# Kernel optimization log

Measured on AMD Instinct MI355X. Metric: run time of the kernel, lower is better.

## Reference

```python
import jax, jax.numpy as jnp
import numpy as np

B, N, D, K = 4, 256, 128, 8
H = 2 * D   # MLP hidden
F3 = 3 * D  # pair feature dim


def setup_inputs() -> dict:
    key = jax.random.key(0)
    ks = jax.random.split(key, 9)
    init = lambda k, shape: (jax.random.normal(k, shape, jnp.float32) * 0.02)
    s = jax.random.normal(ks[0], (B, N, D), jnp.float32)
    return {
        "s": s,
        "Wg1": init(ks[1], (F3, H)), "bg1": jnp.zeros((H,), jnp.float32),
        "Wg2": init(ks[2], (H, 1)),  "bg2": jnp.zeros((1,), jnp.float32),
        "Wa1": init(ks[3], (F3, H)), "ba1": jnp.zeros((H,), jnp.float32),
        "Wa2": init(ks[4], (H, 1)),  "ba2": jnp.zeros((1,), jnp.float32),
    }


def _mlp(x, W1, b1, W2, b2):
    # 2-layer MLP: Linear -> ReLU -> Linear (dropout inactive at eval)
    return jax.nn.relu(x @ W1 + b1) @ W2 + b2


def reference(s, Wg1, bg1, Wg2, bg2, Wa1, ba1, Wa2, ba2):
    b, n, d = s.shape
    si = s[:, :, None, :]                      # [B,N,1,D]
    sj = s[:, None, :, :]                      # [B,1,N,D]
    pair = jnp.concatenate([
        jnp.broadcast_to(si, (b, n, n, d)),
        jnp.broadcast_to(sj, (b, n, n, d)),
        si * sj,
    ], axis=-1)                                # [B,N,N,3D]

    # Stage 1: discrete top-K peer gating
    scores = _mlp(pair, Wg1, bg1, Wg2, bg2)[..., 0]   # [B,N,N]
    k = min(K, n)
    _, topk_idx = jax.lax.top_k(scores, k)            # [B,N,K]
    gate = jax.nn.one_hot(topk_idx, n, dtype=jnp.float32).sum(-2)  # [B,N,N] binary

    # Stage 2: soft relevance weighting over selected peers
    att_logits = _mlp(pair, Wa1, ba1, Wa2, ba2)[..., 0]            # [B,N,N]
    att_logits = jnp.where(gate > 0, att_logits, -jnp.inf)
    att_weights = jnp.nan_to_num(jax.nn.softmax(att_logits, axis=-1))

    ctx = jnp.einsum('bij,bij,bjd->bid', gate, att_weights, s)     # [B,N,D]
    return ctx, gate, att_weights
```

## Files before the change

### kernel.cpp

```cpp
#include <hip/hip_runtime.h>
#include <math.h>

#define B_ 4
#define N_ 256
#define D_ 128
#define H_ 256
#define K_ 8
#define KK 256
#define NJP 64

typedef short v8s __attribute__((ext_vector_type(8)));
typedef float v16f __attribute__((ext_vector_type(16)));

__device__ inline void split_bf16(float x, unsigned short& hi, unsigned short& lo) {
  unsigned u = __float_as_uint(x);
  unsigned uh = u & 0xFFFF0000u;
  hi = (unsigned short)(uh >> 16);
  float r = x - __uint_as_float(uh);
  unsigned ur = __float_as_uint(r);
  ur += 0x7FFFu + ((ur >> 16) & 1u);
  lo = (unsigned short)(ur >> 16);
}

__global__ __launch_bounds__(256) void prep_an(
    const float* __restrict__ s,
    const float* __restrict__ Wg1, const float* __restrict__ bg1,
    const float* __restrict__ Wa1, const float* __restrict__ ba1,
    float* __restrict__ Ag, float* __restrict__ Aa,
    unsigned short* __restrict__ Shi, unsigned short* __restrict__ Slo) {
  const int b = blockIdx.x >> 8;
  const int n = blockIdx.x & 255;
  const int h = threadIdx.x;
  __shared__ float sh[D_];
  if (h < D_) sh[h] = s[(b * N_ + n) * D_ + h];
  __syncthreads();
  float ag = bg1[h], aa = ba1[h];
#pragma unroll 8
  for (int d = 0; d < D_; d++) {
    ag = fmaf(sh[d], Wg1[d * H_ + h], ag);
    aa = fmaf(sh[d], Wa1[d * H_ + h], aa);
  }
  Ag[(b * N_ + n) * H_ + h] = ag;
  Aa[(b * N_ + n) * H_ + h] = aa;
  if (h < D_) {
    unsigned short x, y;
    split_bf16(sh[h], x, y);
    Shi[(b * N_ + n) * D_ + h] = x;
    Slo[(b * N_ + n) * D_ + h] = y;
  }
}

__global__ __launch_bounds__(64) void prep_sw(
    const float* __restrict__ Wg1, const float* __restrict__ Wa1,
    unsigned short* __restrict__ Wghi, unsigned short* __restrict__ Wglo,
    unsigned short* __restrict__ Wahi) {
  const int ks = blockIdx.x >> 3;
  const int tile = blockIdx.x & 7;
  const int lane = threadIdx.x;
  const int h = tile * 32 + (lane & 31);
  const int kbase = ks * 16 + (lane >> 5) * 8;
  const int idx0 = (blockIdx.x * 64 + lane) * 8;
#pragma unroll
  for (int e = 0; e < 8; e++) {
    const int k = kbase + e;
    const int f = (k < D_) ? (2 * D_ + k) : k;
    unsigned short x, y;
    split_bf16(Wg1[f * H_ + h], x, y);
    Wghi[idx0 + e] = x;
    Wglo[idx0 + e] = y;
    unsigned short xa, ya;
    split_bf16(Wa1[f * H_ + h], xa, ya);
    Wahi[idx0 + e] = xa;
  }
}

__global__ __launch_bounds__(256) void prep_sf(
    const unsigned short* __restrict__ Shi, const unsigned short* __restrict__ Slo,
    unsigned short* __restrict__ Sfh, unsigned short* __restrict__ Sfl) {
  const int b = blockIdx.x >> 3, jt = blockIdx.x & 7;
  const int lane = threadIdx.x & 63;
  const int k0 = threadIdx.x >> 6;
  const int j = jt * 32 + (lane & 31);
#pragma unroll
  for (int ksl = k0; ksl < 8; ksl += 4) {
    const int d = ksl * 16 + (lane >> 5) * 8;
    const int src = (b * N_ + j) * D_ + d;
    const int dst = (((b * 8 + jt) * 8 + ksl) * 64 + lane) * 8;
    *(v8s*)(Sfh + dst) = *(const v8s*)(Shi + src);
    *(v8s*)(Sfl + dst) = *(const v8s*)(Slo + src);
  }
}

__device__ inline void arg_better(float v2, int i2, float& v, int& idx) {
  if (v2 > v || (v2 == v && i2 < idx)) { v = v2; idx = i2; }
}

__device__ inline int a_idx(int jl, int k) {
  return (((jl >> 5) * 8 + (k >> 4)) * 64 + ((k >> 3) & 1) * 32 + (jl & 31)) * 8
         + (k & 7);
}
#define ALO 8192

__global__ __launch_bounds__(256, 2) void score_kernel(
    const float* __restrict__ s,
    const float* __restrict__ Ag, const float* __restrict__ Aa,
    const unsigned short* __restrict__ Shi, const unsigned short* __restrict__ Slo,
    const unsigned short* __restrict__ Sfh, const unsigned short* __restrict__ Sfl,
    const unsigned short* __restrict__ Wghi, const unsigned short* __restrict__ Wglo,
    const unsigned short* __restrict__ Wahi,
    const float* __restrict__ Wg2, const float* __restrict__ bg2p,
    const float* __restrict__ Wa2, const float* __restrict__ ba2p,
    float* __restrict__ out) {
  const int b = blockIdx.x >> 8;
  const int i = blockIdx.x & 255;
  const int t = threadIdx.x;
  const int wv = t >> 6, lane = t & 63;
  const int m32 = lane & 31, half32 = lane >> 5;

  __shared__ __align__(16) unsigned short a_all[2 * 8192 + 64];
  __shared__ float si_sh[D_];
  __shared__ float sc_part[8 * NJP];
  __shared__ float scg_sh[N_];
  __shared__ float attl_sh[N_];
  __shared__ float red_v[4];
  __shared__ int red_i[4];
  __shared__ int sel_list[K_];

  if (t < D_) si_sh[t] = s[(b * N_ + i) * D_ + t];

  float agv[2], w2g[2], aav[2], w2a[2];
#pragma unroll
  for (int ht = 0; ht < 2; ht++) {
    const int hg = wv * 64 + ht * 32 + m32;
    agv[ht] = Ag[(b * N_ + i) * H_ + hg];
    w2g[ht] = Wg2[hg];
    aav[ht] = Aa[(b * N_ + i) * H_ + hg];
    w2a[ht] = Wa2[hg];
  }

  const int boff = ((2 * wv) * 64 + lane) * 8;

#pragma unroll 1
  for (int ph = 0; ph < 4; ph++) {
    __syncthreads();
    {
      const int jl = t >> 2, kq = t & 3;
      const int jg = b * N_ + ph * NJP + jl;
      const float* srow = s + jg * D_ + kq * 32;
      const float* sic = si_sh + kq * 32;
#pragma unroll
      for (int u = 0; u < 4; u++) {
        const float4 sv0 = *(const float4*)(srow + u * 8);
        const float4 sv1 = *(const float4*)(srow + u * 8 + 4);
        unsigned short hh[8], ll[8];
        split_bf16(sic[u * 8 + 0] * sv0.x, hh[0], ll[0]);
        split_bf16(sic[u * 8 + 1] * sv0.y, hh[1], ll[1]);
        split_bf16(sic[u * 8 + 2] * sv0.z, hh[2], ll[2]);
        split_bf16(sic[u * 8 + 3] * sv0.w, hh[3], ll[3]);
        split_bf16(sic[u * 8 + 4] * sv1.x, hh[4], ll[4]);
        split_bf16(sic[u * 8 + 5] * sv1.y, hh[5], ll[5]);
        split_bf16(sic[u * 8 + 6] * sv1.z, hh[6], ll[6]);
        split_bf16(sic[u * 8 + 7] * sv1.w, hh[7], ll[7]);
        v8s vh, vl;
#pragma unroll
        for (int e = 0; e < 8; e++) { vh[e] = (short)hh[e]; vl[e] = (short)ll[e]; }
        const int idx = a_idx(jl, kq * 32 + u * 8);
        *(v8s*)(a_all + idx) = vh;
        *(v8s*)(a_all + ALO + idx) = vl;
      }
    }
    __syncthreads();

    const unsigned short* sf_base_h = Sfh + ((b * 8 + ph * 2) * 8) * 512 + lane * 8;
    const unsigned short* sf_base_l = Sfl + ((b * 8 + ph * 2) * 8) * 512 + lane * 8;

    {
      v16f acc[2][2];
#pragma unroll
      for (int jt = 0; jt < 2; jt++)
#pragma unroll
        for (int ht = 0; ht < 2; ht++) acc[jt][ht] = (v16f)(0.f);

      const unsigned short* pgh = Wghi + boff;
      const unsigned short* pgl = Wglo + boff;
      v8s bh[2][2], bl[2][2];
      bh[0][0] = *(const v8s*)pgh;  bh[0][1] = *(const v8s*)(pgh + 512);
      bl[0][0] = *(const v8s*)pgl;  bl[0][1] = *(const v8s*)(pgl + 512);
      pgh += 4096;  pgl += 4096;

      const unsigned short* ahp = a_all + lane * 8;
#pragma unroll 2
      for (int ks = 0; ks < 8; ks++) {
        const int cur = ks & 1, nxt = cur ^ 1;
        bh[nxt][0] = *(const v8s*)pgh;  bh[nxt][1] = *(const v8s*)(pgh + 512);
        bl[nxt][0] = *(const v8s*)pgl;  bl[nxt][1] = *(const v8s*)(pgl + 512);
        pgh += 4096;  pgl += 4096;
        v8s ah0 = *(const v8s*)(ahp);
        v8s ah1 = *(const v8s*)(ahp + 4096);
        v8s al0 = *(const v8s*)(ahp + ALO);
        v8s al1 = *(const v8s*)(ahp + ALO + 4096);
        ahp += 512;
        acc[0][0] = __builtin_amdgcn_mfma_f32_32x32x16_bf16(ah0, bh[cur][0], acc[0][0], 0, 0, 0);
        acc[0][1] = __builtin_amdgcn_mfma_f32_32x32x16_bf16(ah0, bh[cur][1], acc[0][1], 0, 0, 0);
        acc[0][0] = __builtin_amdgcn_mfma_f32_32x32x16_bf16(ah0, bl[cur][0], acc[0][0], 0, 0, 0);
        acc[0][1] = __builtin_amdgcn_mfma_f32_32x32x16_bf16(ah0, bl[cur][1], acc[0][1], 0, 0, 0);
        acc[0][0] = __builtin_amdgcn_mfma_f32_32x32x16_bf16(al0, bh[cur][0], acc[0][0], 0, 0, 0);
        acc[0][1] = __builtin_amdgcn_mfma_f32_32x32x16_bf16(al0, bh[cur][1], acc[0][1], 0, 0, 0);
        acc[1][0] = __builtin_amdgcn_mfma_f32_32x32x16_bf16(ah1, bh[cur][0], acc[1][0], 0, 0, 0);
        acc[1][1] = __builtin_amdgcn_mfma_f32_32x32x16_bf16(ah1, bh[cur][1], acc[1][1], 0, 0, 0);
        acc[1][0] = __builtin_amdgcn_mfma_f32_32x32x16_bf16(ah1, bl[cur][0], acc[1][0], 0, 0, 0);
        acc[1][1] = __builtin_amdgcn_mfma_f32_32x32x16_bf16(ah1, bl[cur][1], acc[1][1], 0, 0, 0);
        acc[1][0] = __builtin_amdgcn_mfma_f32_32x32x16_bf16(al1, bh[cur][0], acc[1][0], 0, 0, 0);
        acc[1][1] = __builtin_amdgcn_mfma_f32_32x32x16_bf16(al1, bh[cur][1], acc[1][1], 0, 0, 0);
      }
      const unsigned short* sfh = sf_base_h;
      const unsigned short* sfl = sf_base_l;
#pragma unroll 2
      for (int ks = 8; ks < 16; ks++) {
        const int cur = ks & 1, nxt = cur ^ 1;
        bh[nxt][0] = *(const v8s*)pgh;  bh[nxt][1] = *(const v8s*)(pgh + 512);
        bl[nxt][0] = *(const v8s*)pgl;  bl[nxt][1] = *(const v8s*)(pgl + 512);
        pgh += 4096;  pgl += 4096;
        v8s ah0 = *(const v8s*)(sfh);
        v8s ah1 = *(const v8s*)(sfh + 4096);
        v8s al0 = *(const v8s*)(sfl);
        v8s al1 = *(const v8s*)(sfl + 4096);
        sfh += 512;  sfl += 512;
        acc[0][0] = __builtin_amdgcn_mfma_f32_32x32x16_bf16(ah0, bh[cur][0], acc[0][0], 0, 0, 0);
        acc[0][1] = __builtin_amdgcn_mfma_f32_32x32x16_bf16(ah0, bh[cur][1], acc[0][1], 0, 0, 0);
        acc[0][0] = __builtin_amdgcn_mfma_f32_32x32x16_bf16(ah0, bl[cur][0], acc[0][0], 0, 0, 0);
        acc[0][1] = __builtin_amdgcn_mfma_f32_32x32x16_bf16(ah0, bl[cur][1], acc[0][1], 0, 0, 0);
        acc[0][0] = __builtin_amdgcn_mfma_f32_32x32x16_bf16(al0, bh[cur][0], acc[0][0], 0, 0, 0);
        acc[0][1] = __builtin_amdgcn_mfma_f32_32x32x16_bf16(al0, bh[cur][1], acc[0][1], 0, 0, 0);
        acc[1][0] = __builtin_amdgcn_mfma_f32_32x32x16_bf16(ah1, bh[cur][0], acc[1][0], 0, 0, 0);
        acc[1][1] = __builtin_amdgcn_mfma_f32_32x32x16_bf16(ah1, bh[cur][1], acc[1][1], 0, 0, 0);
        acc[1][0] = __builtin_amdgcn_mfma_f32_32x32x16_bf16(ah1, bl[cur][0], acc[1][0], 0, 0, 0);
        acc[1][1] = __builtin_amdgcn_mfma_f32_32x32x16_bf16(ah1, bl[cur][1], acc[1][1], 0, 0, 0);
        acc[1][0] = __builtin_amdgcn_mfma_f32_32x32x16_bf16(al1, bh[cur][0], acc[1][0], 0, 0, 0);
        acc[1][1] = __builtin_amdgcn_mfma_f32_32x32x16_bf16(al1, bh[cur][1], acc[1][1], 0, 0, 0);
      }
      float sg[32];
#pragma unroll
      for (int m = 0; m < 32; m++) sg[m] = 0.f;
#pragma unroll
      for (int ht = 0; ht < 2; ht++)
#pragma unroll
        for (int jt = 0; jt < 2; jt++)
#pragma unroll
          for (int r = 0; r < 16; r++) {
            const float z = acc[jt][ht][r] + agv[ht];
            sg[jt * 16 + r] = fmaf(fmaxf(z, 0.f), w2g[ht], sg[jt * 16 + r]);
          }
#pragma unroll
      for (int m = 0; m < 32; m++) {
        float v = sg[m];
#pragma unroll
        for (int off = 1; off <= 16; off <<= 1) v += __shfl_xor(v, off, 64);
        sg[m] = v;
      }
      if (m32 == 0) {
#pragma unroll
        for (int jt = 0; jt < 2; jt++)
#pragma unroll
          for (int r = 0; r < 16; r++) {
            const int jl = jt * 32 + (r & 3) + 8 * (r >> 2) + 4 * half32;
            sc_part[wv * NJP + jl] = sg[jt * 16 + r];
          }
      }
    }

    {
      v16f acc[2][2];
#pragma unroll
      for (int jt = 0; jt < 2; jt++)
#pragma unroll
        for (int ht = 0; ht < 2; ht++) acc[jt][ht] = (v16f)(0.f);

      const unsigned short* pah = Wahi + boff;
      v8s bh[2][2];
      bh[0][0] = *(const v8s*)pah;  bh[0][1] = *(const v8s*)(pah + 512);
      pah += 4096;

      const unsigned short* ahp = a_all + lane * 8;
#pragma unroll 2
      for (int ks = 0; ks < 8; ks++) {
        const int cur = ks & 1, nxt = cur ^ 1;
        bh[nxt][0] = *(const v8s*)pah;  bh[nxt][1] = *(const v8s*)(pah + 512);
        pah += 4096;
        v8s ah0 = *(const v8s*)(ahp);
        v8s ah1 = *(const v8s*)(ahp + 4096);
        ahp += 512;
        acc[0][0] = __builtin_amdgcn_mfma_f32_32x32x16_bf16(ah0, bh[cur][0], acc[0][0], 0, 0, 0);
        acc[0][1] = __builtin_amdgcn_mfma_f32_32x32x16_bf16(ah0, bh[cur][1], acc[0][1], 0, 0, 0);
        acc[1][0] = __builtin_amdgcn_mfma_f32_32x32x16_bf16(ah1, bh[cur][0], acc[1][0], 0, 0, 0);
        acc[1][1] = __builtin_amdgcn_mfma_f32_32x32x16_bf16(ah1, bh[cur][1], acc[1][1], 0, 0, 0);
      }
      const unsigned short* sfh = sf_base_h;
#pragma unroll 2
      for (int ks = 8; ks < 16; ks++) {
        const int cur = ks & 1, nxt = cur ^ 1;
        bh[nxt][0] = *(const v8s*)pah;  bh[nxt][1] = *(const v8s*)(pah + 512);
        pah += 4096;
        v8s ah0 = *(const v8s*)(sfh);
        v8s ah1 = *(const v8s*)(sfh + 4096);
        sfh += 512;
        acc[0][0] = __builtin_amdgcn_mfma_f32_32x32x16_bf16(ah0, bh[cur][0], acc[0][0], 0, 0, 0);
        acc[0][1] = __builtin_amdgcn_mfma_f32_32x32x16_bf16(ah0, bh[cur][1], acc[0][1], 0, 0, 0);
        acc[1][0] = __builtin_amdgcn_mfma_f32_32x32x16_bf16(ah1, bh[cur][0], acc[1][0], 0, 0, 0);
        acc[1][1] = __builtin_amdgcn_mfma_f32_32x32x16_bf16(ah1, bh[cur][1], acc[1][1], 0, 0, 0);
      }
      float sa[32];
#pragma unroll
      for (int m = 0; m < 32; m++) sa[m] = 0.f;
#pragma unroll
      for (int ht = 0; ht < 2; ht++)
#pragma unroll
        for (int jt = 0; jt < 2; jt++)
#pragma unroll
          for (int r = 0; r < 16; r++) {
            const float z = acc[jt][ht][r] + aav[ht];
            sa[jt * 16 + r] = fmaf(fmaxf(z, 0.f), w2a[ht], sa[jt * 16 + r]);
          }
#pragma unroll
      for (int m = 0; m < 32; m++) {
        float v = sa[m];
#pragma unroll
        for (int off = 1; off <= 16; off <<= 1) v += __shfl_xor(v, off, 64);
        sa[m] = v;
      }
      if (m32 == 0) {
#pragma unroll
        for (int jt = 0; jt < 2; jt++)
#pragma unroll
          for (int r = 0; r < 16; r++) {
            const int jl = jt * 32 + (r & 3) + 8 * (r >> 2) + 4 * half32;
            sc_part[4 * NJP + wv * NJP + jl] = sa[jt * 16 + r];
          }
      }
    }
    __syncthreads();
    if (t < NJP) {
      scg_sh[ph * NJP + t] = sc_part[t] + sc_part[NJP + t] + sc_part[2 * NJP + t]
                           + sc_part[3 * NJP + t] + bg2p[0];
      attl_sh[ph * NJP + t] = sc_part[4 * NJP + t] + sc_part[5 * NJP + t]
                            + sc_part[6 * NJP + t] + sc_part[7 * NJP + t] + ba2p[0];
    }
  }
  __syncthreads();

  for (int k = 0; k < K_; k++) {
    float v = scg_sh[t];
    int idx = t;
#pragma unroll
    for (int off = 32; off > 0; off >>= 1) {
      const float vo = __shfl_down(v, off, 64);
      const int io = __shfl_down(idx, off, 64);
      arg_better(vo, io, v, idx);
    }
    if ((t & 63) == 0) { red_v[t >> 6] = v; red_i[t >> 6] = idx; }
    __syncthreads();
    if (t == 0) {
      float bv = red_v[0];
      int bi = red_i[0];
      for (int w = 1; w < 4; w++) arg_better(red_v[w], red_i[w], bv, bi);
      sel_list[k] = bi;
      scg_sh[bi] = -INFINITY;
    }
    __syncthreads();
  }

  bool selj = false;
#pragma unroll
  for (int k = 0; k < K_; k++) selj = selj || (sel_list[k] == t);

  if (t == 0) {
    float m = -INFINITY;
    for (int k = 0; k < K_; k++) m = fmaxf(m, attl_sh[sel_list[k]]);
    float ssum = 0.f;
    for (int k = 0; k < K_; k++) ssum += expf(attl_sh[sel_list[k]] - m);
    red_v[0] = m;
    red_v[1] = ssum;
  }
  __syncthreads();
  const float att = selj ? expf(attl_sh[t] - red_v[0]) / red_v[1] : 0.f;

  float* __restrict__ ctx_out = out;
  float* __restrict__ gate_out = out + B_ * N_ * D_;
  float* __restrict__ att_out = out + B_ * N_ * D_ + B_ * N_ * N_;

  const int row = (b * N_ + i) * N_;
  gate_out[row + t] = selj ? 1.f : 0.f;
  att_out[row + t] = att;

  __syncthreads();
  attl_sh[t] = att;
  __syncthreads();

  if (t < D_) {
    float acc2 = 0.f;
#pragma unroll
    for (int k = 0; k < K_; k++) {
      const int jj = sel_list[k];
      acc2 = fmaf(attl_sh[jj], s[(b * N_ + jj) * D_ + t], acc2);
    }
    ctx_out[(b * N_ + i) * D_ + t] = acc2;
  }
}

extern "C" void kernel_launch(void* const* d_in, const int* in_sizes, int n_in,
                              void* d_out, int out_size, void* d_ws, size_t ws_size,
                              hipStream_t stream) {
  const float* s   = (const float*)d_in[0];
  const float* Wg1 = (const float*)d_in[1];
  const float* bg1 = (const float*)d_in[2];
  const float* Wg2 = (const float*)d_in[3];
  const float* bg2 = (const float*)d_in[4];
  const float* Wa1 = (const float*)d_in[5];
  const float* ba1 = (const float*)d_in[6];
  const float* Wa2 = (const float*)d_in[7];
  const float* ba2 = (const float*)d_in[8];
  float* out = (float*)d_out;

  float* ws = (float*)d_ws;
  float* Ag = ws;
  float* Aa = Ag + B_ * N_ * H_;
  unsigned short* Shi  = (unsigned short*)(Aa + B_ * N_ * H_);
  unsigned short* Slo  = Shi + B_ * N_ * D_;
  unsigned short* Wghi = Slo + B_ * N_ * D_;
  unsigned short* Wglo = Wghi + 65536 + 4096;
  unsigned short* Wahi = Wglo + 65536 + 4096;
  unsigned short* Sfh  = Wahi + 65536 + 4096;
  unsigned short* Sfl  = Sfh + B_ * 32768;

  prep_an<<<dim3(B_ * N_), dim3(256), 0, stream>>>(
      s, Wg1, bg1, Wa1, ba1, Ag, Aa, Shi, Slo);
  prep_sw<<<dim3(128), dim3(64), 0, stream>>>(Wg1, Wa1, Wghi, Wglo, Wahi);
  prep_sf<<<dim3(B_ * 8), dim3(256), 0, stream>>>(Shi, Slo, Sfh, Sfl);
  score_kernel<<<dim3(B_ * N_), dim3(256), 0, stream>>>(
      s, Ag, Aa, Shi, Slo, Sfh, Sfl, Wghi, Wglo, Wahi, Wg2, bg2, Wa2, ba2, out);
}
```

Measured before the change: 264.5 us.

## Process two query rows per score block and merge prep kernels into one

Each score_kernel block now handles two query rows i, so the per-j weight fragments (Wg/Wa hi/lo) and the Sf tiles loaded from global memory are reused across two sets of MFMA accumulators. This halves the grid to 512 blocks and doubles the accumulator registers and shared-memory A buffers. The three prep kernels are fused into a single launch, and the split of s into bf16 hi/lo is done directly from fp32 inside it, removing the Shi/Slo intermediates. The risks are higher register pressure under launch_bounds(256,2), which could cause spills or lower occupancy, and fewer blocks to spread across the CUs.

```diff
diff --git a/kernel.cpp b/kernel.cpp
--- a/kernel.cpp
+++ b/kernel.cpp
@@ -6,7 +6,6 @@
 #define D_ 128
 #define H_ 256
 #define K_ 8
-#define KK 256
 #define NJP 64
 
 typedef short v8s __attribute__((ext_vector_type(8)));
@@ -22,72 +21,73 @@
   lo = (unsigned short)(ur >> 16);
 }
 
-__global__ __launch_bounds__(256) void prep_an(
+__global__ __launch_bounds__(256) void prep_all(
     const float* __restrict__ s,
     const float* __restrict__ Wg1, const float* __restrict__ bg1,
     const float* __restrict__ Wa1, const float* __restrict__ ba1,
     float* __restrict__ Ag, float* __restrict__ Aa,
-    unsigned short* __restrict__ Shi, unsigned short* __restrict__ Slo) {
-  const int b = blockIdx.x >> 8;
-  const int n = blockIdx.x & 255;
-  const int h = threadIdx.x;
+    unsigned short* __restrict__ Wghi, unsigned short* __restrict__ Wglo,
+    unsigned short* __restrict__ Wahi,
+    unsigned short* __restrict__ Sfh, unsigned short* __restrict__ Sfl) {
   __shared__ float sh[D_];
-  if (h < D_) sh[h] = s[(b * N_ + n) * D_ + h];
-  __syncthreads();
-  float ag = bg1[h], aa = ba1[h];
+  const int blk = blockIdx.x;
+  if (blk < 1024) {
+    const int b = blk >> 8, n = blk & 255, h = threadIdx.x;
+    if (h < D_) sh[h] = s[(b * N_ + n) * D_ + h];
+    __syncthreads();
+    float ag = bg1[h], aa = ba1[h];
 #pragma unroll 8
-  for (int d = 0; d < D_; d++) {
-    ag = fmaf(sh[d], Wg1[d * H_ + h], ag);
-    aa = fmaf(sh[d], Wa1[d * H_ + h], aa);
-  }
-  Ag[(b * N_ + n) * H_ + h] = ag;
-  Aa[(b * N_ + n) * H_ + h] = aa;
-  if (h < D_) {
-    unsigned short x, y;
-    split_bf16(sh[h], x, y);
-    Shi[(b * N_ + n) * D_ + h] = x;
-    Slo[(b * N_ + n) * D_ + h] = y;
-  }
-}
-
-__global__ __launch_bounds__(64) void prep_sw(
-    const float* __restrict__ Wg1, const float* __restrict__ Wa1,
-    unsigned short* __restrict__ Wghi, unsigned short* __restrict__ Wglo,
-    unsigned short* __restrict__ Wahi) {
-  const int ks = blockIdx.x >> 3;
-  const int tile = blockIdx.x & 7;
-  const int lane = threadIdx.x;
-  const int h = tile * 32 + (lane & 31);
-  const int kbase = ks * 16 + (lane >> 5) * 8;
-  const int idx0 = (blockIdx.x * 64 + lane) * 8;
-#pragma unroll
-  for (int e = 0; e < 8; e++) {
-    const int k = kbase + e;
-    const int f = (k < D_) ? (2 * D_ + k) : k;
-    unsigned short x, y;
-    split_bf16(Wg1[f * H_ + h], x, y);
-    Wghi[idx0 + e] = x;
-    Wglo[idx0 + e] = y;
-    unsigned short xa, ya;
-    split_bf16(Wa1[f * H_ + h], xa, ya);
-    Wahi[idx0 + e] = xa;
-  }
-}
-
-__global__ __launch_bounds__(256) void prep_sf(
-    const unsigned short* __restrict__ Shi, const unsigned short* __restrict__ Slo,
-    unsigned short* __restrict__ Sfh, unsigned short* __restrict__ Sfl) {
-  const int b = blockIdx.x >> 3, jt = blockIdx.x & 7;
-  const int lane = threadIdx.x & 63;
-  const int k0 = threadIdx.x >> 6;
-  const int j = jt * 32 + (lane & 31);
-#pragma unroll
-  for (int ksl = k0; ksl < 8; ksl += 4) {
-    const int d = ksl * 16 + (lane >> 5) * 8;
-    const int src = (b * N_ + j) * D_ + d;
-    const int dst = (((b * 8 + jt) * 8 + ksl) * 64 + lane) * 8;
-    *(v8s*)(Sfh + dst) = *(const v8s*)(Shi + src);
-    *(v8s*)(Sfl + dst) = *(const v8s*)(Slo + src);
+    for (int d = 0; d < D_; d++) {
+      ag = fmaf(sh[d], Wg1[d * H_ + h], ag);
+      aa = fmaf(sh[d], Wa1[d * H_ + h], aa);
+    }
+    Ag[(b * N_ + n) * H_ + h] = ag;
+    Aa[(b * N_ + n) * H_ + h] = aa;
+  } else if (blk < 1152) {
+    const int id = blk - 1024;
+    if (threadIdx.x < 64) {
+      const int ks = id >> 3, tile = id & 7, lane = threadIdx.x;
+      const int h = tile * 32 + (lane & 31);
+      const int kbase = ks * 16 + (lane >> 5) * 8;
+      const int idx0 = (id * 64 + lane) * 8;
+#pragma unroll
+      for (int e = 0; e < 8; e++) {
+        const int k = kbase + e;
+        const int f = (k < D_) ? (2 * D_ + k) : k;
+        unsigned short x, y;
+        split_bf16(Wg1[f * H_ + h], x, y);
+        Wghi[idx0 + e] = x;
+        Wglo[idx0 + e] = y;
+        unsigned short xa, ya;
+        split_bf16(Wa1[f * H_ + h], xa, ya);
+        Wahi[idx0 + e] = xa;
+      }
+    }
+  } else {
+    const int id = blk - 1152;
+    const int b = id >> 3, jt = id & 7;
+    const int lane = threadIdx.x & 63, k0 = threadIdx.x >> 6;
+    const int j = jt * 32 + (lane & 31);
+#pragma unroll
+    for (int ksl = k0; ksl < 8; ksl += 4) {
+      const int d = ksl * 16 + (lane >> 5) * 8;
+      const float* sp = s + (b * N_ + j) * D_ + d;
+      const float4 f0 = *(const float4*)(sp);
+      const float4 f1 = *(const float4*)(sp + 4);
+      v8s vh, vl;
+      unsigned short x, y;
+      split_bf16(f0.x, x, y); vh[0] = (short)x; vl[0] = (short)y;
+      split_bf16(f0.y, x, y); vh[1] = (short)x; vl[1] = (short)y;
+      split_bf16(f0.z, x, y); vh[2] = (short)x; vl[2] = (short)y;
+      split_bf16(f0.w, x, y); vh[3] = (short)x; vl[3] = (short)y;
+      split_bf16(f1.x, x, y); vh[4] = (short)x; vl[4] = (short)y;
+      split_bf16(f1.y, x, y); vh[5] = (short)x; vl[5] = (short)y;
+      split_bf16(f1.z, x, y); vh[6] = (short)x; vl[6] = (short)y;
+      split_bf16(f1.w, x, y); vh[7] = (short)x; vl[7] = (short)y;
+      const int dst = (((b * 8 + jt) * 8 + ksl) * 64 + lane) * 8;
+      *(v8s*)(Sfh + dst) = vh;
+      *(v8s*)(Sfl + dst) = vl;
+    }
   }
 }
 
@@ -99,46 +99,52 @@
   return (((jl >> 5) * 8 + (k >> 4)) * 64 + ((k >> 3) & 1) * 32 + (jl & 31)) * 8
          + (k & 7);
 }
+#define AI 16384
 #define ALO 8192
 
 __global__ __launch_bounds__(256, 2) void score_kernel(
     const float* __restrict__ s,
     const float* __restrict__ Ag, const float* __restrict__ Aa,
-    const unsigned short* __restrict__ Shi, const unsigned short* __restrict__ Slo,
     const unsigned short* __restrict__ Sfh, const unsigned short* __restrict__ Sfl,
     const unsigned short* __restrict__ Wghi, const unsigned short* __restrict__ Wglo,
     const unsigned short* __restrict__ Wahi,
     const float* __restrict__ Wg2, const float* __restrict__ bg2p,
     const float* __restrict__ Wa2, const float* __restrict__ ba2p,
     float* __restrict__ out) {
-  const int b = blockIdx.x >> 8;
-  const int i = blockIdx.x & 255;
+  const int b = blockIdx.x >> 7;
+  const int q = blockIdx.x & 127;
+  const int i0 = q * 2;
   const int t = threadIdx.x;
   const int wv = t >> 6, lane = t & 63;
   const int m32 = lane & 31, half32 = lane >> 5;
 
-  __shared__ __align__(16) unsigned short a_all[2 * 8192 + 64];
-  __shared__ float si_sh[D_];
-  __shared__ float sc_part[8 * NJP];
-  __shared__ float scg_sh[N_];
-  __shared__ float attl_sh[N_];
+  __shared__ __align__(16) unsigned short a_all[2 * AI + 64];
+  __shared__ float si_sh[2 * D_];
+  __shared__ float sc_part[1024];
+  __shared__ float scg_sh[2 * N_];
+  __shared__ float attl_sh[2 * N_];
   __shared__ float red_v[4];
   __shared__ int red_i[4];
-  __shared__ int sel_list[K_];
-
-  if (t < D_) si_sh[t] = s[(b * N_ + i) * D_ + t];
-
-  float agv[2], w2g[2], aav[2], w2a[2];
+  __shared__ int sel_list[2][K_];
+
+  if (t < 2 * D_) si_sh[t] = s[(b * N_ + i0) * D_ + t];
+
+  float agv[2][2], aav[2][2], w2g[2], w2a[2];
 #pragma unroll
   for (int ht = 0; ht < 2; ht++) {
     const int hg = wv * 64 + ht * 32 + m32;
-    agv[ht] = Ag[(b * N_ + i) * H_ + hg];
     w2g[ht] = Wg2[hg];
-    aav[ht] = Aa[(b * N_ + i) * H_ + hg];
     w2a[ht] = Wa2[hg];
+#pragma unroll
+    for (int ii = 0; ii < 2; ii++) {
+      agv[ii][ht] = Ag[(b * N_ + i0 + ii) * H_ + hg];
+      aav[ii][ht] = Aa[(b * N_ + i0 + ii) * H_ + hg];
+    }
   }
 
   const int boff = ((2 * wv) * 64 + lane) * 8;
+
+#define MF(A_, B_v, C_) C_ = __builtin_amdgcn_mfma_f32_32x32x16_bf16(A_, B_v, C_, 0, 0, 0)
 
 #pragma unroll 1
   for (int ph = 0; ph < 4; ph++) {
@@ -147,26 +153,28 @@
       const int jl = t >> 2, kq = t & 3;
       const int jg = b * N_ + ph * NJP + jl;
       const float* srow = s + jg * D_ + kq * 32;
-      const float* sic = si_sh + kq * 32;
-#pragma unroll
-      for (int u = 0; u < 4; u++) {
-        const float4 sv0 = *(const float4*)(srow + u * 8);
-        const float4 sv1 = *(const float4*)(srow + u * 8 + 4);
-        unsigned short hh[8], ll[8];
-        split_bf16(sic[u * 8 + 0] * sv0.x, hh[0], ll[0]);
-        split_bf16(sic[u * 8 + 1] * sv0.y, hh[1], ll[1]);
-        split_bf16(sic[u * 8 + 2] * sv0.z, hh[2], ll[2]);
-        split_bf16(sic[u * 8 + 3] * sv0.w, hh[3], ll[3]);
-        split_bf16(sic[u * 8 + 4] * sv1.x, hh[4], ll[4]);
-        split_bf16(sic[u * 8 + 5] * sv1.y, hh[5], ll[5]);
-        split_bf16(sic[u * 8 + 6] * sv1.z, hh[6], ll[6]);
-        split_bf16(sic[u * 8 + 7] * sv1.w, hh[7], ll[7]);
-        v8s vh, vl;
-#pragma unroll
-        for (int e = 0; e < 8; e++) { vh[e] = (short)hh[e]; vl[e] = (short)ll[e]; }
-        const int idx = a_idx(jl, kq * 32 + u * 8);
-        *(v8s*)(a_all + idx) = vh;
-        *(v8s*)(a_all + ALO + idx) = vl;
+#pragma unroll
+      for (int ii = 0; ii < 2; ii++) {
+        const float* sic = si_sh + ii * D_ + kq * 32;
+        unsigned short* base = a_all + ii * AI;
+#pragma unroll
+        for (int u = 0; u < 4; u++) {
+          const float4 sv0 = *(const float4*)(srow + u * 8);
+          const float4 sv1 = *(const float4*)(srow + u * 8 + 4);
+          v8s vh, vl;
+          unsigned short x, y;
+          split_bf16(sic[u * 8 + 0] * sv0.x, x, y); vh[0] = (short)x; vl[0] = (short)y;
+          split_bf16(sic[u * 8 + 1] * sv0.y, x, y); vh[1] = (short)x; vl[1] = (short)y;
+          split_bf16(sic[u * 8 + 2] * sv0.z, x, y); vh[2] = (short)x; vl[2] = (short)y;
+          split_bf16(sic[u * 8 + 3] * sv0.w, x, y); vh[3] = (short)x; vl[3] = (short)y;
+          split_bf16(sic[u * 8 + 4] * sv1.x, x, y); vh[4] = (short)x; vl[4] = (short)y;
+          split_bf16(sic[u * 8 + 5] * sv1.y, x, y); vh[5] = (short)x; vl[5] = (short)y;
+          split_bf16(sic[u * 8 + 6] * sv1.z, x, y); vh[6] = (short)x; vl[6] = (short)y;
+          split_bf16(sic[u * 8 + 7] * sv1.w, x, y); vh[7] = (short)x; vl[7] = (short)y;
+          const int idx = a_idx(jl, kq * 32 + u * 8);
+          *(v8s*)(base + idx) = vh;
+          *(v8s*)(base + ALO + idx) = vl;
+        }
       }
     }
     __syncthreads();
@@ -175,11 +183,13 @@
     const unsigned short* sf_base_l = Sfl + ((b * 8 + ph * 2) * 8) * 512 + lane * 8;
 
     {
-      v16f acc[2][2];
-#pragma unroll
-      for (int jt = 0; jt < 2; jt++)
-#pragma unroll
-        for (int ht = 0; ht < 2; ht++) acc[jt][ht] = (v16f)(0.f);
+      v16f acc[2][2][2];
+#pragma unroll
+      for (int ii = 0; ii < 2; ii++)
+#pragma unroll
+        for (int jt = 0; jt < 2; jt++)
+#pragma unroll
+          for (int ht = 0; ht < 2; ht++) acc[ii][jt][ht] = (v16f)(0.f);
 
       const unsigned short* pgh = Wghi + boff;
       const unsigned short* pgl = Wglo + boff;
@@ -195,23 +205,27 @@
         bh[nxt][0] = *(const v8s*)pgh;  bh[nxt][1] = *(const v8s*)(pgh + 512);
         bl[nxt][0] = *(const v8s*)pgl;  bl[nxt][1] = *(const v8s*)(pgl + 512);
         pgh += 4096;  pgl += 4096;
-        v8s ah0 = *(const v8s*)(ahp);
-        v8s ah1 = *(const v8s*)(ahp + 4096);
-        v8s al0 = *(const v8s*)(ahp + ALO);
-        v8s al1 = *(const v8s*)(ahp + ALO + 4096);
+        v8s a0h0 = *(const v8s*)(ahp);
+        v8s a0h1 = *(const v8s*)(ahp + 4096);
+        v8s a0l0 = *(const v8s*)(ahp + ALO);
+        v8s a0l1 = *(const v8s*)(ahp + ALO + 4096);
+        v8s a1h0 = *(const v8s*)(ahp + AI);
+        v8s a1h1 = *(const v8s*)(ahp + AI + 4096);
+        v8s a1l0 = *(const v8s*)(ahp + AI + ALO);
+        v8s a1l1 = *(const v8s*)(ahp + AI + ALO + 4096);
         ahp += 512;
-        acc[0][0] = __builtin_amdgcn_mfma_f32_32x32x16_bf16(ah0, bh[cur][0], acc[0][0], 0, 0, 0);
-        acc[0][1] = __builtin_amdgcn_mfma_f32_32x32x16_bf16(ah0, bh[cur][1], acc[0][1], 0, 0, 0);
-        acc[0][0] = __builtin_amdgcn_mfma_f32_32x32x16_bf16(ah0, bl[cur][0], acc[0][0], 0, 0, 0);
-        acc[0][1] = __builtin_amdgcn_mfma_f32_32x32x16_bf16(ah0, bl[cur][1], acc[0][1], 0, 0, 0);
-        acc[0][0] = __builtin_amdgcn_mfma_f32_32x32x16_bf16(al0, bh[cur][0], acc[0][0], 0, 0, 0);
-        acc[0][1] = __builtin_amdgcn_mfma_f32_32x32x16_bf16(al0, bh[cur][1], acc[0][1], 0, 0, 0);
-        acc[1][0] = __builtin_amdgcn_mfma_f32_32x32x16_bf16(ah1, bh[cur][0], acc[1][0], 0, 0, 0);
-        acc[1][1] = __builtin_amdgcn_mfma_f32_32x32x16_bf16(ah1, bh[cur][1], acc[1][1], 0, 0, 0);
-        acc[1][0] = __builtin_amdgcn_mfma_f32_32x32x16_bf16(ah1, bl[cur][0], acc[1][0], 0, 0, 0);
-        acc[1][1] = __builtin_amdgcn_mfma_f32_32x32x16_bf16(ah1, bl[cur][1], acc[1][1], 0, 0, 0);
-        acc[1][0] = __builtin_amdgcn_mfma_f32_32x32x16_bf16(al1, bh[cur][0], acc[1][0], 0, 0, 0);
-        acc[1][1] = __builtin_amdgcn_mfma_f32_32x32x16_bf16(al1, bh[cur][1], acc[1][1], 0, 0, 0);
+        MF(a0h0, bh[cur][0], acc[0][0][0]); MF(a0h0, bh[cur][1], acc[0][0][1]);
+        MF(a0h0, bl[cur][0], acc[0][0][0]); MF(a0h0, bl[cur][1], acc[0][0][1]);
+        MF(a0l0, bh[cur][0], acc[0][0][0]); MF(a0l0, bh[cur][1], acc[0][0][1]);
+        MF(a0h1, bh[cur][0], acc[0][1][0]); MF(a0h1, bh[cur][1], acc[0][1][1]);
+        MF(a0h1, bl[cur][0], acc[0][1][0]); MF(a0h1, bl[cur][1], acc[0][1][1]);
+        MF(a0l1, bh[cur][0], acc[0][1][0]); MF(a0l1, bh[cur][1], acc[0][1][1]);
+        MF(a1h0, bh[cur][0], acc[1][0][0]); MF(a1h0, bh[cur][1], acc[1][0][1]);
+        MF(a1h0, bl[cur][0], acc[1][0][0]); MF(a1h0, bl[cur][1], acc[1][0][1]);
+        MF(a1l0, bh[cur][0], acc[1][0][0]); MF(a1l0, bh[cur][1], acc[1][0][1]);
+        MF(a1h1, bh[cur][0], acc[1][1][0]); MF(a1h1, bh[cur][1], acc[1][1][1]);
+        MF(a1h1, bl[cur][0], acc[1][1][0]); MF(a1h1, bl[cur][1], acc[1][1][1]);
+        MF(a1l1, bh[cur][0], acc[1][1][0]); MF(a1l1, bh[cur][1], acc[1][1][1]);
       }
       const unsigned short* sfh = sf_base_h;
       const unsigned short* sfl = sf_base_l;
@@ -226,55 +240,57 @@
         v8s al0 = *(const v8s*)(sfl);
         v8s al1 = *(const v8s*)(sfl + 4096);
         sfh += 512;  sfl += 512;
-        acc[0][0] = __builtin_amdgcn_mfma_f32_32x32x16_bf16(ah0, bh[cur][0], acc[0][0], 0, 0, 0);
-        acc[0][1] = __builtin_amdgcn_mfma_f32_32x32x16_bf16(ah0, bh[cur][1], acc[0][1], 0, 0, 0);
-        acc[0][0] = __builtin_amdgcn_mfma_f32_32x32x16_bf16(ah0, bl[cur][0], acc[0][0], 0, 0, 0);
-        acc[0][1] = __builtin_amdgcn_mfma_f32_32x32x16_bf16(ah0, bl[cur][1], acc[0][1], 0, 0, 0);
-        acc[0][0] = __builtin_amdgcn_mfma_f32_32x32x16_bf16(al0, bh[cur][0], acc[0][0], 0, 0, 0);
-        acc[0][1] = __builtin_amdgcn_mfma_f32_32x32x16_bf16(al0, bh[cur][1], acc[0][1], 0, 0, 0);
-        acc[1][0] = __builtin_amdgcn_mfma_f32_32x32x16_bf16(ah1, bh[cur][0], acc[1][0], 0, 0, 0);
-        acc[1][1] = __builtin_amdgcn_mfma_f32_32x32x16_bf16(ah1, bh[cur][1], acc[1][1], 0, 0, 0);
-        acc[1][0] = __builtin_amdgcn_mfma_f32_32x32x16_bf16(ah1, bl[cur][0], acc[1][0], 0, 0, 0);
-        acc[1][1] = __builtin_amdgcn_mfma_f32_32x32x16_bf16(ah1, bl[cur][1], acc[1][1], 0, 0, 0);
-        acc[1][0] = __builtin_amdgcn_mfma_f32_32x32x16_bf16(al1, bh[cur][0], acc[1][0], 0, 0, 0);
-        acc[1][1] = __builtin_amdgcn_mfma_f32_32x32x16_bf16(al1, bh[cur][1], acc[1][1], 0, 0, 0);
-      }
-      float sg[32];
-#pragma unroll
-      for (int m = 0; m < 32; m++) sg[m] = 0.f;
-#pragma unroll
-      for (int ht = 0; ht < 2; ht++)
+#pragma unroll
+        for (int ii = 0; ii < 2; ii++) {
+          MF(ah0, bh[cur][0], acc[ii][0][0]); MF(ah0, bh[cur][1], acc[ii][0][1]);
+          MF(ah0, bl[cur][0], acc[ii][0][0]); MF(ah0, bl[cur][1], acc[ii][0][1]);
+          MF(al0, bh[cur][0], acc[ii][0][0]); MF(al0, bh[cur][1], acc[ii][0][1]);
+          MF(ah1, bh[cur][0], acc[ii][1][0]); MF(ah1, bh[cur][1], acc[ii][1][1]);
+          MF(ah1, bl[cur][0], acc[ii][1][0]); MF(ah1, bl[cur][1], acc[ii][1][1]);
+          MF(al1, bh[cur][0], acc[ii][1][0]); MF(al1, bh[cur][1], acc[ii][1][1]);
+        }
+      }
+#pragma unroll
+      for (int ii = 0; ii < 2; ii++) {
+        float sg[32];
+#pragma unroll
+        for (int m = 0; m < 32; m++) sg[m] = 0.f;
+#pragma unroll
+        for (int ht = 0; ht < 2; ht++)
+#pragma unroll
+          for (int jt = 0; jt < 2; jt++)
+#pragma unroll
+            for (int r = 0; r < 16; r++) {
+              const float z = acc[ii][jt][ht][r] + agv[ii][ht];
+              sg[jt * 16 + r] = fmaf(fmaxf(z, 0.f), w2g[ht], sg[jt * 16 + r]);
+            }
+#pragma unroll
+        for (int m = 0; m < 32; m++) {
+          float v = sg[m];
+#pragma unroll
+          for (int off = 1; off <= 16; off <<= 1) v += __shfl_xor(v, off, 64);
+          sg[m] = v;
+        }
+        if (m32 == 0) {
+#pragma unroll
+          for (int jt = 0; jt < 2; jt++)
+#pragma unroll
+            for (int r = 0; r < 16; r++) {
+              const int jl = jt * 32 + (r & 3) + 8 * (r >> 2) + 4 * half32;
+              sc_part[(ii * 2 + 0) * 256 + wv * NJP + jl] = sg[jt * 16 + r];
+            }
+        }
+      }
+    }
+
+    {
+      v16f acc[2][2][2];
+#pragma unroll
+      for (int ii = 0; ii < 2; ii++)
 #pragma unroll
         for (int jt = 0; jt < 2; jt++)
 #pragma unroll
-          for (int r = 0; r < 16; r++) {
-            const float z = acc[jt][ht][r] + agv[ht];
-            sg[jt * 16 + r] = fmaf(fmaxf(z, 0.f), w2g[ht], sg[jt * 16 + r]);
-          }
-#pragma unroll
-      for (int m = 0; m < 32; m++) {
-        float v = sg[m];
-#pragma unroll
-        for (int off = 1; off <= 16; off <<= 1) v += __shfl_xor(v, off, 64);
-        sg[m] = v;
-      }
-      if (m32 == 0) {
-#pragma unroll
-        for (int jt = 0; jt < 2; jt++)
-#pragma unroll
-          for (int r = 0; r < 16; r++) {
-            const int jl = jt * 32 + (r & 3) + 8 * (r >> 2) + 4 * half32;
-            sc_part[wv * NJP + jl] = sg[jt * 16 + r];
-          }
-      }
-    }
-
-    {
-      v16f acc[2][2];
-#pragma unroll
-      for (int jt = 0; jt < 2; jt++)
-#pragma unroll
-        for (int ht = 0; ht < 2; ht++) acc[jt][ht] = (v16f)(0.f);
+          for (int ht = 0; ht < 2; ht++) acc[ii][jt][ht] = (v16f)(0.f);
 
       const unsigned short* pah = Wahi + boff;
       v8s bh[2][2];
@@ -287,13 +303,15 @@
         const int cur = ks & 1, nxt = cur ^ 1;
         bh[nxt][0] = *(const v8s*)pah;  bh[nxt][1] = *(const v8s*)(pah + 512);
         pah += 4096;
-        v8s ah0 = *(const v8s*)(ahp);
-        v8s ah1 = *(const v8s*)(ahp + 4096);
+        v8s a0h0 = *(const v8s*)(ahp);
+        v8s a0h1 = *(const v8s*)(ahp + 4096);
+        v8s a1h0 = *(const v8s*)(ahp + AI);
+        v8s a1h1 = *(const v8s*)(ahp + AI + 4096);
         ahp += 512;
-        acc[0][0] = __builtin_amdgcn_mfma_f32_32x32x16_bf16(ah0, bh[cur][0], acc[0][0], 0, 0, 0);
-        acc[0][1] = __builtin_amdgcn_mfma_f32_32x32x16_bf16(ah0, bh[cur][1], acc[0][1], 0, 0, 0);
-        acc[1][0] = __builtin_amdgcn_mfma_f32_32x32x16_bf16(ah1, bh[cur][0], acc[1][0], 0, 0, 0);
-        acc[1][1] = __builtin_amdgcn_mfma_f32_32x32x16_bf16(ah1, bh[cur][1], acc[1][1], 0, 0, 0);
+        MF(a0h0, bh[cur][0], acc[0][0][0]); MF(a0h0, bh[cur][1], acc[0][0][1]);
+        MF(a0h1, bh[cur][0], acc[0][1][0]); MF(a0h1, bh[cur][1], acc[0][1][1]);
+        MF(a1h0, bh[cur][0], acc[1][0][0]); MF(a1h0, bh[cur][1], acc[1][0][1]);
+        MF(a1h1, bh[cur][0], acc[1][1][0]); MF(a1h1, bh[cur][1], acc[1][1][1]);
       }
       const unsigned short* sfh = sf_base_h;
 #pragma unroll 2
@@ -304,107 +322,126 @@
         v8s ah0 = *(const v8s*)(sfh);
         v8s ah1 = *(const v8s*)(sfh + 4096);
         sfh += 512;
-        acc[0][0] = __builtin_amdgcn_mfma_f32_32x32x16_bf16(ah0, bh[cur][0], acc[0][0], 0, 0, 0);
-        acc[0][1] = __builtin_amdgcn_mfma_f32_32x32x16_bf16(ah0, bh[cur][1], acc[0][1], 0, 0, 0);
-        acc[1][0] = __builtin_amdgcn_mfma_f32_32x32x16_bf16(ah1, bh[cur][0], acc[1][0], 0, 0, 0);
-        acc[1][1] = __builtin_amdgcn_mfma_f32_32x32x16_bf16(ah1, bh[cur][1], acc[1][1], 0, 0, 0);
-      }
-      float sa[32];
-#pragma unroll
-      for (int m = 0; m < 32; m++) sa[m] = 0.f;
-#pragma unroll
-      for (int ht = 0; ht < 2; ht++)
-#pragma unroll
-        for (int jt = 0; jt < 2; jt++)
-#pragma unroll
-          for (int r = 0; r < 16; r++) {
-            const float z = acc[jt][ht][r] + aav[ht];
-            sa[jt * 16 + r] = fmaf(fmaxf(z, 0.f), w2a[ht], sa[jt * 16 + r]);
-          }
-#pragma unroll
-      for (int m = 0; m < 32; m++) {
-        float v = sa[m];
-#pragma unroll
-        for (int off = 1; off <= 16; off <<= 1) v += __shfl_xor(v, off, 64);
-        sa[m] = v;
-      }
-      if (m32 == 0) {
-#pragma unroll
-        for (int jt = 0; jt < 2; jt++)
-#pragma unroll
-          for (int r = 0; r < 16; r++) {
-            const int jl = jt * 32 + (r & 3) + 8 * (r >> 2) + 4 * half32;
-            sc_part[4 * NJP + wv * NJP + jl] = sa[jt * 16 + r];
-          }
-      }
-    }
-    __syncthreads();
-    if (t < NJP) {
-      scg_sh[ph * NJP + t] = sc_part[t] + sc_part[NJP + t] + sc_part[2 * NJP + t]
-                           + sc_part[3 * NJP + t] + bg2p[0];
-      attl_sh[ph * NJP + t] = sc_part[4 * NJP + t] + sc_part[5 * NJP + t]
-                            + sc_part[6 * NJP + t] + sc_part[7 * NJP + t] + ba2p[0];
+#pragma unroll
+        for (int ii = 0; ii < 2; ii++) {
+          MF(ah0, bh[cur][0], acc[ii][0][0]); MF(ah0, bh[cur][1], acc[ii][0][1]);
+          MF(ah1, bh[cur][0], acc[ii][1][0]); MF(ah1, bh[cur][1], acc[ii][1][1]);
+        }
+      }
+#pragma unroll
+      for (int ii = 0; ii < 2; ii++) {
+        float sa[32];
+#pragma unroll
+        for (int m = 0; m < 32; m++) sa[m] = 0.f;
+#pragma unroll
+        for (int ht = 0; ht < 2; ht++)
+#pragma unroll
+          for (int jt = 0; jt < 2; jt++)
+#pragma unroll
+            for (int r = 0; r < 16; r++) {
+              const float z = acc[ii][jt][ht][r] + aav[ii][ht];
+              sa[jt * 16 + r] = fmaf(fmaxf(z, 0.f), w2a[ht], sa[jt * 16 + r]);
+            }
+#pragma unroll
+        for (int m = 0; m < 32; m++) {
+          float v = sa[m];
+#pragma unroll
+          for (int off = 1; off <= 16; off <<= 1) v += __shfl_xor(v, off, 64);
+          sa[m] = v;
+        }
+        if (m32 == 0) {
+#pragma unroll
+          for (int jt = 0; jt < 2; jt++)
+#pragma unroll
+            for (int r = 0; r < 16; r++) {
+              const int jl = jt * 32 + (r & 3) + 8 * (r >> 2) + 4 * half32;
+              sc_part[(ii * 2 + 1) * 256 + wv * NJP + jl] = sa[jt * 16 + r];
+            }
+        }
+      }
+    }
+    __syncthreads();
+    if (t < 2 * NJP) {
+      const int ii = t >> 6, jl = t & 63;
+      float g = bg2p[0], a = ba2p[0];
+#pragma unroll
+      for (int w = 0; w < 4; w++) {
+        g += sc_part[(ii * 2 + 0) * 256 + w * NJP + jl];
+        a += sc_part[(ii * 2 + 1) * 256 + w * NJP + jl];
+      }
+      scg_sh[ii * N_ + ph * NJP + jl] = g;
+      attl_sh[ii * N_ + ph * NJP + jl] = a;
     }
   }
   __syncthreads();
 
-  for (int k = 0; k < K_; k++) {
-    float v = scg_sh[t];
-    int idx = t;
-#pragma unroll
-    for (int off = 32; off > 0; off >>= 1) {
-      const float vo = __shfl_down(v, off, 64);
-      const int io = __shfl_down(idx, off, 64);
-      arg_better(vo, io, v, idx);
-    }
-    if ((t & 63) == 0) { red_v[t >> 6] = v; red_i[t >> 6] = idx; }
-    __syncthreads();
-    if (t == 0) {
-      float bv = red_v[0];
-      int bi = red_i[0];
-      for (int w = 1; w < 4; w++) arg_better(red_v[w], red_i[w], bv, bi);
-      sel_list[k] = bi;
-      scg_sh[bi] = -INFINITY;
-    }
-    __syncthreads();
-  }
-
-  bool selj = false;
-#pragma unroll
-  for (int k = 0; k < K_; k++) selj = selj || (sel_list[k] == t);
-
-  if (t == 0) {
-    float m = -INFINITY;
-    for (int k = 0; k < K_; k++) m = fmaxf(m, attl_sh[sel_list[k]]);
-    float ssum = 0.f;
-    for (int k = 0; k < K_; k++) ssum += expf(attl_sh[sel_list[k]] - m);
-    red_v[0] = m;
-    red_v[1] = ssum;
-  }
-  __syncthreads();
-  const float att = selj ? expf(attl_sh[t] - red_v[0]) / red_v[1] : 0.f;
+#pragma unroll 1
+  for (int ii = 0; ii < 2; ii++) {
+    for (int k = 0; k < K_; k++) {
+      float v = scg_sh[ii * N_ + t];
+      int idx = t;
+#pragma unroll
+      for (int off = 32; off > 0; off >>= 1) {
+        const float vo = __shfl_down(v, off, 64);
+        const int io = __shfl_down(idx, off, 64);
+        arg_better(vo, io, v, idx);
+      }
+      if (lane == 0) { red_v[wv] = v; red_i[wv] = idx; }
+      __syncthreads();
+      if (t == 0) {
+        float bv = red_v[0];
+        int bi = red_i[0];
+        for (int w = 1; w < 4; w++) arg_better(red_v[w], red_i[w], bv, bi);
+        sel_list[ii][k] = bi;
+        scg_sh[ii * N_ + bi] = -INFINITY;
+      }
+      __syncthreads();
+    }
+  }
 
   float* __restrict__ ctx_out = out;
   float* __restrict__ gate_out = out + B_ * N_ * D_;
   float* __restrict__ att_out = out + B_ * N_ * D_ + B_ * N_ * N_;
 
-  const int row = (b * N_ + i) * N_;
-  gate_out[row + t] = selj ? 1.f : 0.f;
-  att_out[row + t] = att;
-
-  __syncthreads();
-  attl_sh[t] = att;
-  __syncthreads();
+#pragma unroll 1
+  for (int ii = 0; ii < 2; ii++) {
+    bool selj = false;
+#pragma unroll
+    for (int k = 0; k < K_; k++) selj = selj || (sel_list[ii][k] == t);
+
+    if (t == 0) {
+      float m = -INFINITY;
+      for (int k = 0; k < K_; k++) m = fmaxf(m, attl_sh[ii * N_ + sel_list[ii][k]]);
+      float ssum = 0.f;
+      for (int k = 0; k < K_; k++) ssum += expf(attl_sh[ii * N_ + sel_list[ii][k]] - m);
+      red_v[0] = m;
+      red_v[1] = ssum;
+    }
+    __syncthreads();
+    const float att = selj ? expf(attl_sh[ii * N_ + t] - red_v[0]) / red_v[1] : 0.f;
+
+    const int row = (b * N_ + i0 + ii) * N_;
+    gate_out[row + t] = selj ? 1.f : 0.f;
+    att_out[row + t] = att;
+
+    __syncthreads();
+    attl_sh[ii * N_ + t] = att;
+    __syncthreads();
+  }
 
   if (t < D_) {
-    float acc2 = 0.f;
-#pragma unroll
-    for (int k = 0; k < K_; k++) {
-      const int jj = sel_list[k];
-      acc2 = fmaf(attl_sh[jj], s[(b * N_ + jj) * D_ + t], acc2);
-    }
-    ctx_out[(b * N_ + i) * D_ + t] = acc2;
-  }
+#pragma unroll 1
+    for (int ii = 0; ii < 2; ii++) {
+      float acc2 = 0.f;
+#pragma unroll
+      for (int k = 0; k < K_; k++) {
+        const int jj = sel_list[ii][k];
+        acc2 = fmaf(attl_sh[ii * N_ + jj], s[(b * N_ + jj) * D_ + t], acc2);
+      }
+      ctx_out[(b * N_ + i0 + ii) * D_ + t] = acc2;
+    }
+  }
+#undef MF
 }
 
 extern "C" void kernel_launch(void* const* d_in, const int* in_sizes, int n_in,
@@ -424,18 +461,14 @@
   float* ws = (float*)d_ws;
   float* Ag = ws;
   float* Aa = Ag + B_ * N_ * H_;
-  unsigned short* Shi  = (unsigned short*)(Aa + B_ * N_ * H_);
-  unsigned short* Slo  = Shi + B_ * N_ * D_;
-  unsigned short* Wghi = Slo + B_ * N_ * D_;
+  unsigned short* Wghi = (unsigned short*)(Aa + B_ * N_ * H_);
   unsigned short* Wglo = Wghi + 65536 + 4096;
   unsigned short* Wahi = Wglo + 65536 + 4096;
   unsigned short* Sfh  = Wahi + 65536 + 4096;
   unsigned short* Sfl  = Sfh + B_ * 32768;
 
-  prep_an<<<dim3(B_ * N_), dim3(256), 0, stream>>>(
-      s, Wg1, bg1, Wa1, ba1, Ag, Aa, Shi, Slo);
-  prep_sw<<<dim3(128), dim3(64), 0, stream>>>(Wg1, Wa1, Wghi, Wglo, Wahi);
-  prep_sf<<<dim3(B_ * 8), dim3(256), 0, stream>>>(Shi, Slo, Sfh, Sfl);
-  score_kernel<<<dim3(B_ * N_), dim3(256), 0, stream>>>(
-      s, Ag, Aa, Shi, Slo, Sfh, Sfl, Wghi, Wglo, Wahi, Wg2, bg2, Wa2, ba2, out);
-}
+  prep_all<<<dim3(1184), dim3(256), 0, stream>>>(
+      s, Wg1, bg1, Wa1, ba1, Ag, Aa, Wghi, Wglo, Wahi, Sfh, Sfl);
+  score_kernel<<<dim3(B_ * 128), dim3(256), 0, stream>>>(
+      s, Ag, Aa, Sfh, Sfl, Wghi, Wglo, Wahi, Wg2, bg2, Wa2, ba2, out);
+}
```

Measured after the change: 248.4 us. 6.1% less time.
